# Kernel tuning notes

Measured on AMD Instinct MI355X. Metric: run time of the kernel, lower is better.

Reference implementation:

```python
import jax, jax.numpy as jnp
import numpy as np

FRACTAL_OUTPUT = (5, 5)            # (a, b); requires 5 * num_kernels == a*b
PERC_THRESHOLD = 0.59275
NEXT_SHAPE = (224, 224)
K_END = int(0.4 * FRACTAL_OUTPUT[0] * FRACTAL_OUTPUT[1] + 1)   # 11
KERNEL_SIZES = list(range(3, K_END + 1, 2))                    # [3,5,7,9,11]


def setup_inputs() -> dict:
    key = jax.random.key(0)
    inputs = jax.random.uniform(key, (64, 224, 224, 3), dtype=jnp.float32) * 255.0
    return {"inputs": inputs}


def _extract_patches(x, k):
    # tf.image.extract_patches(sizes=strides=k, SAME) == zero-pad + space-to-depth
    B, H, W, C = x.shape
    rows, cols = -(-H // k), -(-W // k)
    ph, pw = rows * k - H, cols * k - W
    x = jnp.pad(x, ((0, 0), (ph // 2, ph - ph // 2), (pw // 2, pw - pw // 2), (0, 0)))
    x = x.reshape(B, rows, k, cols, k, C).transpose(0, 1, 3, 2, 4, 5)
    return x.reshape(B * rows * cols, k, k, C), rows * cols


def _binarize(patches, k, ch):
    # distance function: 1 iff |channel value - center pixel channel value| <= k
    center = patches[:, k // 2, k // 2, ch][:, None, None]
    return (jnp.abs(patches[..., ch] - center) <= k).astype(jnp.int32)


def _connected_stats(binp, k):
    # 4-connected components via min-label propagation (== tfa connected_components
    # up to relabeling; we only need #components and max label count incl. background)
    N = binp.shape[0]
    idx = jnp.arange(1, k * k + 1, dtype=jnp.int32).reshape(k, k)
    INF = jnp.int32(k * k + 2)
    lbl0 = jnp.where(binp > 0, idx, 0)

    def step(_, lbl):
        v = jnp.where(binp > 0, lbl, INF)
        pad = lambda a, w: jnp.pad(a, ((0, 0),) + w, constant_values=INF)
        up    = pad(v, ((1, 0), (0, 0)))[:, :-1, :]
        down  = pad(v, ((0, 1), (0, 0)))[:, 1:, :]
        left  = pad(v, ((0, 0), (1, 0)))[:, :, :-1]
        right = pad(v, ((0, 0), (0, 1)))[:, :, 1:]
        m = jnp.minimum(jnp.minimum(v, up), jnp.minimum(jnp.minimum(down, left), right))
        return jnp.where(binp > 0, m, 0)

    lbl = jax.lax.fori_loop(0, k * k, step, lbl0)  # k*k iters guarantee convergence
    ncomp = jnp.sum((binp > 0) & (lbl == idx), axis=(1, 2)).astype(jnp.int32)
    lblf = lbl.reshape(N, k * k)
    cnt = jnp.zeros((N, k * k + 1), jnp.int32).at[jnp.arange(N)[:, None], lblf].add(1)
    return ncomp, cnt.max(axis=1)  # (#components, most-common label count incl bg 0)


def _components(inputs, k, ch):
    B = inputs.shape[0]
    patches, P = _extract_patches(inputs, k)
    binp = _binarize(patches, k, ch)                    # (B*P, k, k)
    ones = binp.sum(axis=(1, 2)).reshape(B, P)          # int counts per patch
    # tf.bincount(minlength=1, maxlength=k*k): bins 0..k*k-1, value k*k dropped
    cnt = jnp.zeros((B, k * k + 1), jnp.float32).at[jnp.arange(B)[:, None], ones].add(1.0)
    prob = cnt[:, : k * k] / P                          # (B, k*k)
    n = jnp.arange(1, k * k + 1, dtype=jnp.float32)
    fd = (prob / n).sum(1)
    m = (prob * n).sum(1)
    m2 = ((prob * prob) * n).sum(1)
    lac = (m2 - m * m) / (m * m)
    perc = ((ones.astype(jnp.float32) / (k * k)) >= PERC_THRESHOLD).astype(jnp.int32)
    acp = perc.sum(1) // P                              # tf integer reduce_mean
    ncomp, marea = _connected_stats(binp, k)
    acn = ncomp.reshape(B, P).sum(1) // P
    acma = marea.reshape(B, P).sum(1) // P
    return jnp.stack([acn.astype(jnp.float32), acp.astype(jnp.float32),
                      acma.astype(jnp.float32), lac, fd], axis=1)   # (B, 5)


def _rearrange(c):
    # group metric-major: all acn over kernels, then acp, acma, lac, fd
    return jnp.concatenate([c[:, mm::5] for mm in range(5)], axis=1)


def reference(inputs):
    B = inputs.shape[0]
    chans = []
    for ch in range(3):
        comps = jnp.concatenate([_components(inputs, k, ch) for k in KERNEL_SIZES], axis=1)
        chans.append(_rearrange(comps).reshape(B, FRACTAL_OUTPUT[0], FRACTAL_OUTPUT[1]))
    out = jnp.stack(chans, axis=3)                      # (B, a, b, 3)
    return jax.image.resize(out, (B, NEXT_SHAPE[0], NEXT_SHAPE[1], 3), method='bilinear')
```

## Files before the change

### kernel.cpp

```cpp
#include <hip/hip_runtime.h>

#define HW 224
#define NIMG 64
#define NPIX ((size_t)NIMG * HW * HW)
#define NSLICE 8
#define ACC_STRIDE 128
#define NCOMBO (NIMG * 15)
#define ACC_BYTES (NCOMBO * ACC_STRIDE * 4)

typedef unsigned long long u64;

struct U128 { u64 lo, hi; };

__device__ __forceinline__ u64  u_or  (u64 a, u64 b){ return a | b; }
__device__ __forceinline__ u64  u_and (u64 a, u64 b){ return a & b; }
__device__ __forceinline__ u64  u_andn(u64 a, u64 b){ return a & ~b; }
__device__ __forceinline__ bool u_eq(u64 a, u64 b){ return a == b; }
__device__ __forceinline__ bool u_nz(u64 a){ return a != 0ull; }
__device__ __forceinline__ u64  u_shl(u64 a, int n){ return a << n; }
__device__ __forceinline__ u64  u_shr(u64 a, int n){ return a >> n; }
__device__ __forceinline__ int  u_pop(u64 a){ return __popcll(a); }
__device__ __forceinline__ u64  u_low(u64 a){ return a & (0ull - a); }

__device__ __forceinline__ U128 u_or  (U128 a, U128 b){ return {a.lo|b.lo, a.hi|b.hi}; }
__device__ __forceinline__ U128 u_and (U128 a, U128 b){ return {a.lo&b.lo, a.hi&b.hi}; }
__device__ __forceinline__ U128 u_andn(U128 a, U128 b){ return {a.lo&~b.lo, a.hi&~b.hi}; }
__device__ __forceinline__ bool u_eq(U128 a, U128 b){ return a.lo==b.lo && a.hi==b.hi; }
__device__ __forceinline__ bool u_nz(U128 a){ return (a.lo | a.hi) != 0ull; }
__device__ __forceinline__ U128 u_shl(U128 a, int n){
    return { a.lo << n, (a.hi << n) | (a.lo >> (64 - n)) };
}
__device__ __forceinline__ U128 u_shr(U128 a, int n){
    return { (a.lo >> n) | (a.hi << (64 - n)), a.hi >> n };
}
__device__ __forceinline__ int u_pop(U128 a){ return __popcll(a.lo) + __popcll(a.hi); }
__device__ __forceinline__ U128 u_low(U128 a){
    if (a.lo) return { a.lo & (0ull - a.lo), 0ull };
    return { 0ull, a.hi & (0ull - a.hi) };
}

template<bool B, class T, class F> struct sel        { using type = T; };
template<class T, class F>         struct sel<false, T, F> { using type = F; };

template<int K>
__device__ __forceinline__ void load_row(const float* __restrict__ p, float* r) {
#pragma unroll
    for (int j = 0; j + 4 <= K; j += 4) {
        float4 v; __builtin_memcpy(&v, p + j, 16);
        r[j] = v.x; r[j + 1] = v.y; r[j + 2] = v.z; r[j + 3] = v.w;
    }
    if constexpr ((K & 3) >= 2) {
        constexpr int b = (K / 4) * 4;
        float2 v; __builtin_memcpy(&v, p + b, 8);
        r[b] = v.x; r[b + 1] = v.y;
    }
    if constexpr (K & 1) r[K - 1] = p[K - 1];
}

template<int K, int S, class M>
__device__ __forceinline__ void do_patch(const float* __restrict__ img, int p,
                                         M leftCol, M rightCol,
                                         int* hist, int& t_perc, int& t_ncomp,
                                         int& t_marea) {
    constexpr int KK   = K * K;
    constexpr int ROWS = (HW + K - 1) / K;
    constexpr int PAD  = (ROWS * K - HW) / 2;

    const int pr = p / ROWS, pc = p - pr * ROWS;
    const int y0 = pr * K - PAD, x0 = pc * K - PAD;
    const float cen = img[((size_t)(y0 + K / 2) * HW + (x0 + K / 2)) * S];

    M msk;
    if constexpr (KK <= 64) msk = 0ull; else msk = U128{0, 0};

    const bool fast = (S == 1) && (y0 >= 0) && (x0 >= 0) &&
                      (y0 + K <= HW) && (x0 + K <= HW);
    if (fast) {
#pragma unroll
        for (int i = 0; i < K; i++) {
            float r[K];
            load_row<K>(img + (size_t)(y0 + i) * HW + x0, r);
#pragma unroll
            for (int j = 0; j < K; j++) {
                const u64 bit = (fabsf(r[j] - cen) <= (float)K) ? 1ull : 0ull;
                const int cb = i * K + j;
                if constexpr (KK <= 64) msk |= bit << cb;
                else { if (cb < 64) msk.lo |= bit << cb; else msk.hi |= bit << (cb - 64); }
            }
        }
    } else {
#pragma unroll
        for (int i = 0; i < K; i++) {
            const int y = y0 + i;
            const bool yin = (unsigned)y < (unsigned)HW;
#pragma unroll
            for (int j = 0; j < K; j++) {
                const int x = x0 + j;
                const bool inb = yin && ((unsigned)x < (unsigned)HW);
                const float v = inb ? img[((size_t)y * HW + x) * S] : 0.0f;
                const u64 bit = (fabsf(v - cen) <= (float)K) ? 1ull : 0ull;
                const int cb = i * K + j;
                if constexpr (KK <= 64) msk |= bit << cb;
                else { if (cb < 64) msk.lo |= bit << cb; else msk.hi |= bit << (cb - 64); }
            }
        }
    }
    const int ones = u_pop(msk);

    M nbm = u_or(u_or(u_shl(u_andn(msk, rightCol), 1),
                      u_shr(u_andn(msk, leftCol ), 1)),
                 u_or(u_shl(msk, K), u_shr(msk, K)));
    M iso = u_andn(msk, nbm);
    const int niso = u_pop(iso);
    int ncomp = niso, maxsz = (niso > 0) ? 1 : 0;
    M m = u_andn(msk, iso);
    while (u_nz(m)) {
        M s = u_low(m);
        for (;;) {
            M g = u_or(s, u_or(u_or(u_shl(u_andn(s, rightCol), 1),
                                    u_shr(u_andn(s, leftCol ), 1)),
                               u_or(u_shl(s, K), u_shr(s, K))));
            g = u_and(g, m);
            if (u_eq(g, s)) break;
            s = g;
        }
        ncomp++;
        const int sz = u_pop(s);
        if (sz > maxsz) maxsz = sz;
        m = u_andn(m, s);
    }

    const int bgcnt = KK - ones;
    const int marea = (bgcnt > maxsz) ? bgcnt : maxsz;
    t_ncomp += ncomp;
    t_marea += marea;
    if ((float)ones / (float)KK >= 0.59275f) t_perc++;
    atomicAdd(&hist[ones], 1);
}

template<int K>
__device__ __forceinline__ void make_colmasks(u64& lcl, u64& lch, u64& rcl, u64& rch) {
    lcl = lch = rcl = rch = 0;
#pragma unroll
    for (int i = 0; i < K; i++) {
        const int cl = i * K, cr = i * K + K - 1;
        if (cl < 64) lcl |= 1ull << cl; else lch |= 1ull << (cl - 64);
        if (cr < 64) rcl |= 1ull << cr; else rch |= 1ull << (cr - 64);
    }
}

template<int K, int S>
__device__ __forceinline__ void stats_body(const float* __restrict__ img,
                                           int slice, int* hist,
                                           int* __restrict__ gout) {
    constexpr int KK   = K * K;
    constexpr int ROWS = (HW + K - 1) / K;
    constexpr int P    = ROWS * ROWS;
    using M = typename sel<(KK <= 64), u64, U128>::type;

    u64 lcl, lch, rcl, rch;
    make_colmasks<K>(lcl, lch, rcl, rch);
    M leftCol, rightCol;
    if constexpr (KK <= 64) { leftCol = lcl; rightCol = rcl; }
    else { leftCol = U128{lcl, lch}; rightCol = U128{rcl, rch}; }

    for (int s = threadIdx.x; s <= KK; s += 64) hist[s] = 0;
    __syncthreads();

    const int pstart = (slice * P) / NSLICE;
    const int pend   = ((slice + 1) * P) / NSLICE;

    int t_perc = 0, t_ncomp = 0, t_marea = 0;
    for (int p = pstart + threadIdx.x; p < pend; p += 64)
        do_patch<K, S, M>(img, p, leftCol, rightCol, hist, t_perc, t_ncomp, t_marea);

#pragma unroll
    for (int off = 32; off; off >>= 1) {
        t_perc  += __shfl_down(t_perc,  off);
        t_ncomp += __shfl_down(t_ncomp, off);
        t_marea += __shfl_down(t_marea, off);
    }
    __syncthreads();

    for (int s = threadIdx.x; s <= KK; s += 64) {
        const int v = hist[s];
        if (v) atomicAdd(&gout[s], v);
    }
    if (threadIdx.x == 0) {
        atomicAdd(&gout[124], t_perc);
        atomicAdd(&gout[125], t_ncomp);
        atomicAdd(&gout[126], t_marea);
    }
}

template<int S>
__global__ __launch_bounds__(64) void fractal_stats(const float* __restrict__ in,
                                                    int* __restrict__ gacc) {
    const int B     = blockIdx.x;
    const int x     = B & 7;
    const int j     = B >> 3;
    const int gl    = j / 40;
    const int inner = j - gl * 40;
    const int g     = gl * 8 + x;
    const int b     = g / 3, ch = g - b * 3;
    const int kidx  = inner >> 3;
    const int slice = inner & 7;

    __shared__ int hist[124];

    const float* img = (S == 1) ? in + ((size_t)ch * NIMG + b) * HW * HW
                                : in + (size_t)b * HW * HW * 3 + ch;
    int* gout = gacc + (g * 5 + kidx) * ACC_STRIDE;

    switch (kidx) {
        case 0: stats_body<3,  S>(img, slice, hist, gout); break;
        case 1: stats_body<5,  S>(img, slice, hist, gout); break;
        case 2: stats_body<7,  S>(img, slice, hist, gout); break;
        case 3: stats_body<9,  S>(img, slice, hist, gout); break;
        case 4: stats_body<11, S>(img, slice, hist, gout); break;
    }
}

__global__ __launch_bounds__(64) void fractal_finalize(const int* __restrict__ gacc,
                                                       float* __restrict__ interm) {
    const int cidx = blockIdx.x * 64 + threadIdx.x;
    if (cidx >= NCOMBO) return;
    const int b    = cidx / 15;
    const int rem  = cidx % 15;
    const int ch   = rem / 5;
    const int kidx = rem % 5;
    const int K    = 3 + 2 * kidx;
    const int ROWS = (HW + K - 1) / K;
    const int P    = ROWS * ROWS;
    const int KK   = K * K;

    const int* a = gacc + cidx * ACC_STRIDE;
    const float Pf = (float)P;
    float fd = 0.0f, m1 = 0.0f, m2 = 0.0f;
    for (int s = 0; s < KK; s++) {
        const float prob = (float)a[s] / Pf;
        const float n = (float)(s + 1);
        fd += prob / n;
        m1 += prob * n;
        m2 += prob * prob * n;
    }
    const float lac = (m2 - m1 * m1) / (m1 * m1);

    float* o = interm + (size_t)b * 75 + kidx * 3 + ch;
    o[0]  = (float)(a[125] / P);
    o[15] = (float)(a[124] / P);
    o[30] = (float)(a[126] / P);
    o[45] = lac;
    o[60] = fd;
}

template<int K, int S>
__device__ __forceinline__ void stats_body_full(const float* __restrict__ img,
                                                float* __restrict__ o,
                                                int hist4[4][124], int* sums) {
    constexpr int KK   = K * K;
    constexpr int ROWS = (HW + K - 1) / K;
    constexpr int P    = ROWS * ROWS;
    using M = typename sel<(KK <= 64), u64, U128>::type;
    const int wid = threadIdx.x >> 6;

    u64 lcl, lch, rcl, rch;
    make_colmasks<K>(lcl, lch, rcl, rch);
    M leftCol, rightCol;
    if constexpr (KK <= 64) { leftCol = lcl; rightCol = rcl; }
    else { leftCol = U128{lcl, lch}; rightCol = U128{rcl, rch}; }

    int t_perc = 0, t_ncomp = 0, t_marea = 0;
    for (int p = threadIdx.x; p < P; p += 256)
        do_patch<K, S, M>(img, p, leftCol, rightCol, hist4[wid],
                          t_perc, t_ncomp, t_marea);

    atomicAdd(&sums[0], t_perc);
    atomicAdd(&sums[1], t_ncomp);
    atomicAdd(&sums[2], t_marea);
    __syncthreads();

    if (threadIdx.x == 0) {
        const float Pf = (float)P;
        float fd = 0.0f, m1 = 0.0f, m2 = 0.0f;
        for (int s = 0; s < KK; s++) {
            const float prob = (float)(hist4[0][s] + hist4[1][s] + hist4[2][s] + hist4[3][s]) / Pf;
            const float n = (float)(s + 1);
            fd += prob / n;
            m1 += prob * n;
            m2 += prob * prob * n;
        }
        const float lac = (m2 - m1 * m1) / (m1 * m1);
        o[0]  = (float)(sums[1] / P);
        o[15] = (float)(sums[0] / P);
        o[30] = (float)(sums[2] / P);
        o[45] = lac;
        o[60] = fd;
    }
}

template<int S>
__global__ __launch_bounds__(256) void fractal_stats_full(const float* __restrict__ in,
                                                          float* __restrict__ interm) {
    const int b    = blockIdx.x / 15;
    const int rem  = blockIdx.x % 15;
    const int ch   = rem / 5;
    const int kidx = rem % 5;

    __shared__ int hist[4][124];
    __shared__ int sums[3];
    for (int i = threadIdx.x; i < 4 * 124; i += 256) ((int*)hist)[i] = 0;
    if (threadIdx.x < 3) sums[threadIdx.x] = 0;
    __syncthreads();

    const float* img = in + (size_t)b * HW * HW * 3 + ch;
    float* o = interm + (size_t)b * 75 + kidx * 3 + ch;

    switch (kidx) {
        case 0: stats_body_full<3,  S>(img, o, hist, sums); break;
        case 1: stats_body_full<5,  S>(img, o, hist, sums); break;
        case 2: stats_body_full<7,  S>(img, o, hist, sums); break;
        case 3: stats_body_full<9,  S>(img, o, hist, sums); break;
        case 4: stats_body_full<11, S>(img, o, hist, sums); break;
    }
}

__global__ __launch_bounds__(256) void deinterleave(const float* __restrict__ in,
                                                    float* __restrict__ planes,
                                                    int* __restrict__ gacc) {
    const int t = blockIdx.x * 256 + threadIdx.x;
    if (t < ACC_BYTES / 16) {
        const int4 z = make_int4(0, 0, 0, 0);
        ((int4*)gacc)[t] = z;
    }
    const size_t pix = (size_t)t * 4;
    if (pix >= NPIX) return;
    float4 a, b, c;
    __builtin_memcpy(&a, in + pix * 3,     16);
    __builtin_memcpy(&b, in + pix * 3 + 4, 16);
    __builtin_memcpy(&c, in + pix * 3 + 8, 16);
    const float4 p0 = make_float4(a.x, a.w, b.z, c.y);
    const float4 p1 = make_float4(a.y, b.x, b.w, c.z);
    const float4 p2 = make_float4(a.z, b.y, c.x, c.w);
    __builtin_memcpy(planes + pix,            &p0, 16);
    __builtin_memcpy(planes + NPIX + pix,     &p1, 16);
    __builtin_memcpy(planes + 2 * NPIX + pix, &p2, 16);
}

__global__ __launch_bounds__(256) void fractal_resize(const float* __restrict__ interm,
                                                      float* __restrict__ out, int total) {
    const int idx = blockIdx.x * 256 + threadIdx.x;
    if (idx >= total) return;
    const int ch = idx % 3;
    int t = idx / 3;
    const int x = t % HW; t /= HW;
    const int y = t % HW;
    const int b = t / HW;

    const float sc = 5.0f / 224.0f;
    const float uy = ((float)y + 0.5f) * sc - 0.5f;
    const float ux = ((float)x + 0.5f) * sc - 0.5f;

    const float fy = floorf(uy), fx = floorf(ux);
    const float wy = uy - fy,    wx = ux - fx;
    int y0 = (int)fy, x0 = (int)fx;
    int y1 = y0 + 1,  x1 = x0 + 1;
    if (y0 < 0) y0 = 0; if (x0 < 0) x0 = 0;
    if (y1 > 4) y1 = 4; if (x1 > 4) x1 = 4;

    const float* g = interm + (size_t)b * 75 + ch;
    const float v00 = g[(y0 * 5 + x0) * 3];
    const float v01 = g[(y0 * 5 + x1) * 3];
    const float v10 = g[(y1 * 5 + x0) * 3];
    const float v11 = g[(y1 * 5 + x1) * 3];

    out[idx] = (1.0f - wy) * ((1.0f - wx) * v00 + wx * v01)
             +         wy  * ((1.0f - wx) * v10 + wx * v11);
}

extern "C" void kernel_launch(void* const* d_in, const int* in_sizes, int n_in,
                              void* d_out, int out_size, void* d_ws, size_t ws_size,
                              hipStream_t stream) {
    const float* in = (const float*)d_in[0];
    float* out = (float*)d_out;
    float* interm = (float*)d_ws;

    const size_t acc_off    = 19456;
    const size_t planes_off = acc_off + ACC_BYTES;
    const size_t need = planes_off + 3 * NPIX * sizeof(float);

    if (ws_size >= need) {
        int*   gacc   = (int*)((char*)d_ws + acc_off);
        float* planes = (float*)((char*)d_ws + planes_off);
        deinterleave<<<(int)(NPIX / 4 / 256), 256, 0, stream>>>(in, planes, gacc);
        fractal_stats<1><<<192 * 40, 64, 0, stream>>>(planes, gacc);
        fractal_finalize<<<(NCOMBO + 63) / 64, 64, 0, stream>>>(gacc, interm);
    } else {
        fractal_stats_full<3><<<NIMG * 15, 256, 0, stream>>>(in, interm);
    }
    fractal_resize<<<(out_size + 255) / 256, 256, 0, stream>>>(interm, out, out_size);
}
```

Baseline: 164.5 us.

## Rebalance stats work into per-wave patch chunks and simplify resize indexing

The stats kernel moves from 64-thread blocks, each handling one eighth of the patches for a kernel size, to 256-thread blocks whose four waves take fixed-size patch chunks sized per kernel. This gives 60 jobs per image-channel, intended to balance the uneven per-patch cost across sizes. The shared-memory histogram and its block syncs are dropped, so each patch now does a global atomicAdd on its histogram bin, which adds atomic contention. The resize kernel now uses a 2D grid with one thread per pixel writing all three channels, which removes the integer div/mod work.

```diff
diff --git a/kernel.cpp b/kernel.cpp
--- a/kernel.cpp
+++ b/kernel.cpp
@@ -3,7 +3,6 @@
 #define HW 224
 #define NIMG 64
 #define NPIX ((size_t)NIMG * HW * HW)
-#define NSLICE 8
 #define ACC_STRIDE 128
 #define NCOMBO (NIMG * 15)
 #define ACC_BYTES (NCOMBO * ACC_STRIDE * 4)
@@ -60,7 +59,7 @@
 template<int K, int S, class M>
 __device__ __forceinline__ void do_patch(const float* __restrict__ img, int p,
                                          M leftCol, M rightCol,
-                                         int* hist, int& t_perc, int& t_ncomp,
+                                         int* bins, int& t_perc, int& t_ncomp,
                                          int& t_marea) {
     constexpr int KK   = K * K;
     constexpr int ROWS = (HW + K - 1) / K;
@@ -135,7 +134,7 @@
     t_ncomp += ncomp;
     t_marea += marea;
     if ((float)ones / (float)KK >= 0.59275f) t_perc++;
-    atomicAdd(&hist[ones], 1);
+    atomicAdd(&bins[ones], 1);
 }
 
 template<int K>
@@ -150,12 +149,13 @@
 }
 
 template<int K, int S>
-__device__ __forceinline__ void stats_body(const float* __restrict__ img,
-                                           int slice, int* hist,
-                                           int* __restrict__ gout) {
-    constexpr int KK   = K * K;
+__device__ __forceinline__ void job_body(const float* __restrict__ img,
+                                         int chunk, int lane,
+                                         int* __restrict__ gout) {
     constexpr int ROWS = (HW + K - 1) / K;
     constexpr int P    = ROWS * ROWS;
+    constexpr int PPJ  = (K == 3) ? 512 : (K == 5 ? 128 : 64);
+    constexpr int KK   = K * K;
     using M = typename sel<(KK <= 64), u64, U128>::type;
 
     u64 lcl, lch, rcl, rch;
@@ -164,15 +164,13 @@
     if constexpr (KK <= 64) { leftCol = lcl; rightCol = rcl; }
     else { leftCol = U128{lcl, lch}; rightCol = U128{rcl, rch}; }
 
-    for (int s = threadIdx.x; s <= KK; s += 64) hist[s] = 0;
-    __syncthreads();
-
-    const int pstart = (slice * P) / NSLICE;
-    const int pend   = ((slice + 1) * P) / NSLICE;
+    const int pstart = chunk * PPJ;
+    const int pend   = (pstart + PPJ < P) ? (pstart + PPJ) : P;
 
     int t_perc = 0, t_ncomp = 0, t_marea = 0;
-    for (int p = pstart + threadIdx.x; p < pend; p += 64)
-        do_patch<K, S, M>(img, p, leftCol, rightCol, hist, t_perc, t_ncomp, t_marea);
+    for (int p = pstart + lane; p < pend; p += 64)
+        do_patch<K, S, M>(img, p, leftCol, rightCol, gout,
+                          t_perc, t_ncomp, t_marea);
 
 #pragma unroll
     for (int off = 32; off; off >>= 1) {
@@ -180,13 +178,7 @@
         t_ncomp += __shfl_down(t_ncomp, off);
         t_marea += __shfl_down(t_marea, off);
     }
-    __syncthreads();
-
-    for (int s = threadIdx.x; s <= KK; s += 64) {
-        const int v = hist[s];
-        if (v) atomicAdd(&gout[s], v);
-    }
-    if (threadIdx.x == 0) {
+    if (lane == 0) {
         atomicAdd(&gout[124], t_perc);
         atomicAdd(&gout[125], t_ncomp);
         atomicAdd(&gout[126], t_marea);
@@ -194,30 +186,34 @@
 }
 
 template<int S>
-__global__ __launch_bounds__(64) void fractal_stats(const float* __restrict__ in,
-                                                    int* __restrict__ gacc) {
-    const int B     = blockIdx.x;
-    const int x     = B & 7;
-    const int j     = B >> 3;
-    const int gl    = j / 40;
-    const int inner = j - gl * 40;
-    const int g     = gl * 8 + x;
-    const int b     = g / 3, ch = g - b * 3;
-    const int kidx  = inner >> 3;
-    const int slice = inner & 7;
-
-    __shared__ int hist[124];
+__global__ __launch_bounds__(256) void fractal_stats(const float* __restrict__ in,
+                                                     int* __restrict__ gacc) {
+    const int wave = threadIdx.x >> 6;
+    const int lane = threadIdx.x & 63;
+    const int x    = blockIdx.x & 7;
+    const int j    = blockIdx.x >> 3;
+    const int gl   = j / 15, ib = j - gl * 15;
+    const int g    = gl * 8 + x;
+    const int b    = g / 3, ch = g - b * 3;
+    const int jw   = ib * 4 + wave;
+
+    int kidx, chunk;
+    if      (jw < 11) { kidx = 0; chunk = jw;      }
+    else if (jw < 27) { kidx = 1; chunk = jw - 11; }
+    else if (jw < 43) { kidx = 2; chunk = jw - 27; }
+    else if (jw < 53) { kidx = 3; chunk = jw - 43; }
+    else              { kidx = 4; chunk = jw - 53; }
 
     const float* img = (S == 1) ? in + ((size_t)ch * NIMG + b) * HW * HW
                                 : in + (size_t)b * HW * HW * 3 + ch;
     int* gout = gacc + (g * 5 + kidx) * ACC_STRIDE;
 
     switch (kidx) {
-        case 0: stats_body<3,  S>(img, slice, hist, gout); break;
-        case 1: stats_body<5,  S>(img, slice, hist, gout); break;
-        case 2: stats_body<7,  S>(img, slice, hist, gout); break;
-        case 3: stats_body<9,  S>(img, slice, hist, gout); break;
-        case 4: stats_body<11, S>(img, slice, hist, gout); break;
+        case 0: job_body<3,  S>(img, chunk, lane, gout); break;
+        case 1: job_body<5,  S>(img, chunk, lane, gout); break;
+        case 2: job_body<7,  S>(img, chunk, lane, gout); break;
+        case 3: job_body<9,  S>(img, chunk, lane, gout); break;
+        case 4: job_body<11, S>(img, chunk, lane, gout); break;
     }
 }
 
@@ -349,13 +345,9 @@
 
 __global__ __launch_bounds__(256) void fractal_resize(const float* __restrict__ interm,
                                                       float* __restrict__ out, int total) {
-    const int idx = blockIdx.x * 256 + threadIdx.x;
-    if (idx >= total) return;
-    const int ch = idx % 3;
-    int t = idx / 3;
-    const int x = t % HW; t /= HW;
-    const int y = t % HW;
-    const int b = t / HW;
+    const int x = threadIdx.x;
+    if (x >= HW) return;
+    const int y = blockIdx.x, b = blockIdx.y;
 
     const float sc = 5.0f / 224.0f;
     const float uy = ((float)y + 0.5f) * sc - 0.5f;
@@ -368,14 +360,19 @@
     if (y0 < 0) y0 = 0; if (x0 < 0) x0 = 0;
     if (y1 > 4) y1 = 4; if (x1 > 4) x1 = 4;
 
-    const float* g = interm + (size_t)b * 75 + ch;
-    const float v00 = g[(y0 * 5 + x0) * 3];
-    const float v01 = g[(y0 * 5 + x1) * 3];
-    const float v10 = g[(y1 * 5 + x0) * 3];
-    const float v11 = g[(y1 * 5 + x1) * 3];
-
-    out[idx] = (1.0f - wy) * ((1.0f - wx) * v00 + wx * v01)
-             +         wy  * ((1.0f - wx) * v10 + wx * v11);
+    const float w00 = (1.0f - wy) * (1.0f - wx), w01 = (1.0f - wy) * wx;
+    const float w10 = wy * (1.0f - wx),          w11 = wy * wx;
+
+    const float* gp = interm + (size_t)b * 75;
+    const int base = ((b * HW + y) * HW + x) * 3;
+    if (base + 3 > total) return;
+#pragma unroll
+    for (int ch = 0; ch < 3; ch++) {
+        out[base + ch] = w00 * gp[(y0 * 5 + x0) * 3 + ch]
+                       + w01 * gp[(y0 * 5 + x1) * 3 + ch]
+                       + w10 * gp[(y1 * 5 + x0) * 3 + ch]
+                       + w11 * gp[(y1 * 5 + x1) * 3 + ch];
+    }
 }
 
 extern "C" void kernel_launch(void* const* d_in, const int* in_sizes, int n_in,
@@ -393,10 +390,10 @@
         int*   gacc   = (int*)((char*)d_ws + acc_off);
         float* planes = (float*)((char*)d_ws + planes_off);
         deinterleave<<<(int)(NPIX / 4 / 256), 256, 0, stream>>>(in, planes, gacc);
-        fractal_stats<1><<<192 * 40, 64, 0, stream>>>(planes, gacc);
+        fractal_stats<1><<<2880, 256, 0, stream>>>(planes, gacc);
         fractal_finalize<<<(NCOMBO + 63) / 64, 64, 0, stream>>>(gacc, interm);
     } else {
         fractal_stats_full<3><<<NIMG * 15, 256, 0, stream>>>(in, interm);
     }
-    fractal_resize<<<(out_size + 255) / 256, 256, 0, stream>>>(interm, out, out_size);
-}
+    fractal_resize<<<dim3(HW, NIMG), 256, 0, stream>>>(interm, out, out_size);
+}
```

Measured after the change: 305.4 us. +85.7%, slower.
